# Kernel optimization log

Hardware: AMD Instinct MI355X
Metric: run time of the kernel (lower is better)

## Reference

```python
import jax, jax.numpy as jnp
import numpy as np

N = 100000
E = 1600000
D_IN = 128
D_H = 128


def setup_inputs() -> dict:
    key = jax.random.key(0)
    ks = jax.random.split(key, 8)
    x = jax.random.normal(ks[0], (N, D_IN), dtype=jnp.float32)
    edge_index = jax.random.randint(ks[1], (2, E), 0, N, dtype=jnp.int64)
    # Glorot-ish init for weights, zeros for biases (PyG GCNConv default: glorot W, zero bias)
    W1 = jax.random.normal(ks[2], (D_IN, D_H), dtype=jnp.float32) / np.sqrt(D_IN)
    b1 = jnp.zeros((D_H,), dtype=jnp.float32)
    W2 = jax.random.normal(ks[3], (D_H, D_H), dtype=jnp.float32) / np.sqrt(D_H)
    b2 = jnp.zeros((D_H,), dtype=jnp.float32)
    Wout = jax.random.normal(ks[4], (D_H, 1), dtype=jnp.float32) / np.sqrt(D_H)
    bout = jnp.zeros((1,), dtype=jnp.float32)
    return {"x": x, "edge_index": edge_index, "W1": W1, "b1": b1,
            "W2": W2, "b2": b2, "Wout": Wout, "bout": bout}


def _gcn_conv(x, W, b, src, dst, inv_sqrt_deg, inv_deg):
    # PyG GCNConv: h = x @ W; out = sum_{j in N(i)} norm_ij * h_j + (1/deg_i) * h_i + b
    # norm_ij = deg_i^-1/2 * deg_j^-1/2 with self-loops folded into deg.
    h = x @ W                                   # [N, D]
    norm = inv_sqrt_deg[src] * inv_sqrt_deg[dst]  # [E]
    msgs = h[src] * norm[:, None]               # [E, D] gather
    agg = jax.ops.segment_sum(msgs, dst, num_segments=x.shape[0])  # [N, D] scatter
    agg = agg + h * inv_deg[:, None]            # self-loop term (norm = 1/deg)
    return agg + b


def reference(x, edge_index, W1, b1, W2, b2, Wout, bout):
    src = edge_index[0]
    dst = edge_index[1]
    n = x.shape[0]
    # degree with self-loops: deg_i = 1 + #incoming edges to i
    deg = 1.0 + jax.ops.segment_sum(jnp.ones((src.shape[0],), dtype=x.dtype), dst, num_segments=n)
    inv_sqrt_deg = jax.lax.rsqrt(deg)
    inv_deg = 1.0 / deg
    h = jax.nn.relu(_gcn_conv(x, W1, b1, src, dst, inv_sqrt_deg, inv_deg))
    h = jax.nn.relu(_gcn_conv(h, W2, b2, src, dst, inv_sqrt_deg, inv_deg))
    logits = h @ Wout + bout                    # [N, 1]
    return jax.nn.sigmoid(logits).squeeze(-1)   # [N]
```

## Files before the change

kernel.cpp:

```cpp
#include <hip/hip_runtime.h>
#include <cstddef>

#define CAPD 64
#define BSZ 512
#define BSH 9
#define CHUNK 8192
#define BCAP 12288

typedef unsigned int uint;
typedef unsigned short ushort;
typedef unsigned char uchar;
typedef float f32x4 __attribute__((ext_vector_type(4)));
typedef _Float16 f16x8 __attribute__((ext_vector_type(8)));

__device__ inline float h_lo(uint v) {
    union { ushort u; _Float16 h; } c; c.u = (ushort)(v & 0xFFFFu); return (float)c.h;
}
__device__ inline float h_hi(uint v) {
    union { ushort u; _Float16 h; } c; c.u = (ushort)(v >> 16); return (float)c.h;
}
__device__ inline ushort h_bits(float x) {
    union { _Float16 h; ushort u; } c; c.h = (_Float16)x; return c.u;
}
__device__ inline uint h_pack(float a, float b) {
    return (uint)h_bits(a) | ((uint)h_bits(b) << 16);
}
__device__ inline float ub0(uint v) { return (float)(v & 0xFFu); }
__device__ inline float ub1(uint v) { return (float)((v >> 8) & 0xFFu); }
__device__ inline float ub2(uint v) { return (float)((v >> 16) & 0xFFu); }
__device__ inline float ub3(uint v) { return (float)(v >> 24); }

__global__ __launch_bounds__(256) void p3_scatter(const int* __restrict__ esrc,
                                                  const int* __restrict__ edst, int E,
                                                  int nb, int NB2,
                                                  int* __restrict__ bucketCursor,
                                                  unsigned* __restrict__ gSorted,
                                                  const float* __restrict__ W1,
                                                  const float* __restrict__ W2,
                                                  uint* __restrict__ Wt1,
                                                  uint* __restrict__ Wt2) {
    __shared__ __align__(16) char SHB[78848];
    int bid = blockIdx.x, tid = threadIdx.x;
    if (bid >= NB2) {
        const float* W = (bid - NB2) ? W2 : W1;
        uint* O = (bid - NB2) ? Wt2 : Wt1;
        float (*ws)[129] = (float(*)[129])SHB;
#pragma unroll
        for (int j = 0; j < 16; ++j) {
            int q = tid + 256 * j;
            int k = q >> 5, c = (q & 31) * 4;
            float4 v = *reinterpret_cast<const float4*>(W + k * 128 + c);
            ws[k][c] = v.x; ws[k][c + 1] = v.y; ws[k][c + 2] = v.z; ws[k][c + 3] = v.w;
        }
        __syncthreads();
#pragma unroll
        for (int j = 0; j < 32; ++j) {
            int q = tid + 256 * j;
            int ncol = q >> 6, kw = q & 63;
            O[q] = h_pack(ws[2 * kw][ncol], ws[2 * kw + 1][ncol]);
        }
        return;
    }
    uint*  payL = (uint*)SHB;
    uint*  outL = (uint*)(SHB + 32768);
    uchar* bktL = (uchar*)(SHB + 65536);
    int*   hist   = (int*)(SHB + 73728);
    int*   segoff = hist + 256;
    int*   cursor = segoff + 256;
    int*   gbase  = cursor + 256;
    int*   sc     = gbase + 256;
    int e0 = bid * CHUNK;
    int m = min(E - e0, CHUNK);
    for (int i = tid; i < m; i += 256) {
        unsigned d = (unsigned)edst[e0 + i];
        unsigned s = (unsigned)esrc[e0 + i];
        payL[i] = s | ((d & (BSZ - 1)) << 23);
        bktL[i] = (uchar)(d >> BSH);
    }
    hist[tid] = 0;
    __syncthreads();
    for (int i = tid; i < m; i += 256)
        atomicAdd(&hist[bktL[i]], 1);
    __syncthreads();
    sc[tid] = hist[tid];
    __syncthreads();
    for (int off = 1; off < 256; off <<= 1) {
        int v = (tid >= off) ? sc[tid - off] : 0;
        __syncthreads();
        sc[tid] += v;
        __syncthreads();
    }
    segoff[tid] = sc[tid] - hist[tid];
    cursor[tid] = segoff[tid];
    if (tid < nb && hist[tid] > 0) gbase[tid] = atomicAdd(&bucketCursor[tid], hist[tid]);
    __syncthreads();
    for (int i = tid; i < m; i += 256) {
        int b = (int)bktL[i];
        int p = atomicAdd(&cursor[b], 1);
        outL[p] = payL[i];
    }
    __syncthreads();
    int wave = tid >> 6, lane = tid & 63;
    for (int b = wave; b < nb; b += 4) {
        int off = segoff[b], len = hist[b];
        if (len == 0) continue;
        int gb = gbase[b];
        unsigned* dst = gSorted + (size_t)b * BCAP;
        for (int i = lane; i < len; i += 64)
            if (gb + i < BCAP) dst[gb + i] = outL[off + i];
    }
}

__global__ __launch_bounds__(256) void p4_build(const unsigned* __restrict__ gSorted,
                                                const int* __restrict__ bucketCursor,
                                                int nb, int N, int* __restrict__ cnt,
                                                float* __restrict__ isd,
                                                int* __restrict__ ell) {
    __shared__ unsigned ellL[128 * CAPD];
    __shared__ int cntL[128];
    int bid = blockIdx.x, tid = threadIdx.x;
    int bucket = bid >> 2;
    unsigned sub = (unsigned)(bid & 3);
    int n0 = bid * 128;
    int nValid = min(128, N - n0);
    if (nValid <= 0) return;
    for (int i = tid; i < 128; i += 256) cntL[i] = 0;
    __syncthreads();
    int len = bucketCursor[bucket];
    if (len > BCAP) len = BCAP;
    const unsigned* seg = gSorted + (size_t)bucket * BCAP;
    for (int i = tid; i < len; i += 256) {
        unsigned e = seg[i];
        unsigned dl = e >> 23;
        if ((dl >> 7) == sub) {
            int r = (int)(dl & 127u);
            int p = atomicAdd(&cntL[r], 1);
            if (p < CAPD) ellL[r * CAPD + p] = e & 0x7FFFFFu;
        }
    }
    __syncthreads();
    int total = nValid * CAPD;
    const int* ellLi = (const int*)ellL;
    for (int i = tid; i < total; i += 256) {
        int row = i >> 6, pos = i & 63;
        int c = cntL[row];
        if (pos < min(c, CAPD))
            ell[(size_t)n0 * CAPD + i] = ellLi[i];
    }
    for (int i = tid; i < nValid; i += 256) {
        int c = cntL[i];
        cnt[n0 + i] = c;
        isd[n0 + i] = rsqrtf(1.0f + (float)c);
    }
}

__device__ __forceinline__ void gemm_core(const void* __restrict__ A, int aF16,
                                          const uint* __restrict__ Wt,
                                          const float* __restrict__ scale,
                                          const float* __restrict__ isdT,
                                          uint* __restrict__ Tq,
                                          float* __restrict__ Ts,
                                          float* __restrict__ TscOut,
                                          int n, int m0, int tid, uint* SH) {
    char* shb = (char*)SH;
    if (aF16) {
        const uint* Af = (const uint*)A;
#pragma unroll
        for (int j = 0; j < 8; ++j) {
            int q = tid + 256 * j;
            int row = q >> 4, c16 = q & 15;
            int grow = m0 + row;
            uint4 v = make_uint4(0u, 0u, 0u, 0u);
            if (grow < n) v = *reinterpret_cast<const uint4*>(Af + (size_t)grow * 64 + c16 * 4);
            *reinterpret_cast<uint4*>(shb + row * 256 + ((c16 * 16) ^ ((row & 7) << 4))) = v;
        }
    } else {
        const float* Af = (const float*)A;
#pragma unroll
        for (int j = 0; j < 8; ++j) {
            int q = tid + 256 * j;
            int row = q >> 4, c16 = q & 15;
            int grow = m0 + row;
            uint4 o = make_uint4(0u, 0u, 0u, 0u);
            if (grow < n) {
                float4 v0 = *reinterpret_cast<const float4*>(Af + (size_t)grow * 128 + c16 * 8);
                float4 v1 = *reinterpret_cast<const float4*>(Af + (size_t)grow * 128 + c16 * 8 + 4);
                o.x = h_pack(v0.x, v0.y); o.y = h_pack(v0.z, v0.w);
                o.z = h_pack(v1.x, v1.y); o.w = h_pack(v1.z, v1.w);
            }
            *reinterpret_cast<uint4*>(shb + row * 256 + ((c16 * 16) ^ ((row & 7) << 4))) = o;
        }
    }
#pragma unroll
    for (int j = 0; j < 8; ++j) {
        int q = tid + 256 * j;
        int col = q >> 4, c16 = q & 15;
        uint4 v = *reinterpret_cast<const uint4*>(Wt + col * 64 + c16 * 4);
        *reinterpret_cast<uint4*>(shb + 32768 + col * 256 + ((c16 * 16) ^ ((col & 7) << 4))) = v;
    }
    __syncthreads();

    const int w = tid >> 6, l = tid & 63;
    const int lrow = l & 15, kg = l >> 4;
    const int swz = (lrow & 7) << 4;

    f32x4 acc[2][8] = {};
#pragma unroll
    for (int kk = 0; kk < 4; ++kk) {
        const int koff = (kk * 64 + kg * 16) ^ swz;
        f16x8 a[2], b[8];
#pragma unroll
        for (int mr = 0; mr < 2; ++mr) {
            int r = w * 32 + mr * 16 + lrow;
            a[mr] = *reinterpret_cast<const f16x8*>(shb + r * 256 + koff);
        }
#pragma unroll
        for (int nc = 0; nc < 8; ++nc) {
            int c = nc * 16 + lrow;
            b[nc] = *reinterpret_cast<const f16x8*>(shb + 32768 + c * 256 + koff);
        }
#pragma unroll
        for (int mr = 0; mr < 2; ++mr)
#pragma unroll
            for (int nc = 0; nc < 8; ++nc)
                acc[mr][nc] = __builtin_amdgcn_mfma_f32_16x16x32_f16(a[mr], b[nc], acc[mr][nc], 0, 0, 0);
    }
    __syncthreads();

    ushort* Cs = (ushort*)SH;
#pragma unroll
    for (int mr = 0; mr < 2; ++mr) {
        int rb = w * 32 + mr * 16 + kg * 4;
#pragma unroll
        for (int i = 0; i < 4; ++i) {
            int grow = m0 + rb + i;
            float s = scale ? ((grow < n) ? scale[grow] : 0.f) : 1.f;
#pragma unroll
            for (int nc = 0; nc < 8; ++nc)
                Cs[(rb + i) * 136 + nc * 16 + lrow] = h_bits(s * acc[mr][nc][i]);
        }
    }
    __syncthreads();
    const uint* Cw = (const uint*)SH;
#pragma unroll
    for (int j = 0; j < 8; ++j) {
        int q = tid + 256 * j;
        int row = q >> 4, c8 = q & 15;
        int grow = m0 + row;
        uint4 v = *reinterpret_cast<const uint4*>(Cw + row * 68 + c8 * 4);
        float f0 = h_lo(v.x), f1 = h_hi(v.x), f2 = h_lo(v.y), f3 = h_hi(v.y);
        float f4 = h_lo(v.z), f5 = h_hi(v.z), f6 = h_lo(v.w), f7 = h_hi(v.w);
        float mx = fmaxf(fmaxf(fmaxf(fabsf(f0), fabsf(f1)), fmaxf(fabsf(f2), fabsf(f3))),
                         fmaxf(fmaxf(fabsf(f4), fabsf(f5)), fmaxf(fabsf(f6), fabsf(f7))));
#pragma unroll
        for (int off = 8; off > 0; off >>= 1) mx = fmaxf(mx, __shfl_xor(mx, off, 16));
        mx = fmaxf(mx, 1e-20f);
        float inv = 127.f / mx;
        int q0 = (int)rintf(f0 * inv) + 128, q1 = (int)rintf(f1 * inv) + 128;
        int q2 = (int)rintf(f2 * inv) + 128, q3 = (int)rintf(f3 * inv) + 128;
        int q4 = (int)rintf(f4 * inv) + 128, q5 = (int)rintf(f5 * inv) + 128;
        int q6 = (int)rintf(f6 * inv) + 128, q7 = (int)rintf(f7 * inv) + 128;
        uint w0 = (uint)q0 | ((uint)q1 << 8) | ((uint)q2 << 16) | ((uint)q3 << 24);
        uint w1 = (uint)q4 | ((uint)q5 << 8) | ((uint)q6 << 16) | ((uint)q7 << 24);
        if (grow < n) {
            *reinterpret_cast<uint2*>(Tq + (size_t)grow * 32 + c8 * 2) = make_uint2(w0, w1);
            if (c8 == 0) {
                float ts = mx * (1.f / 127.f);
                Ts[grow] = ts;
                if (TscOut) TscOut[grow] = ts * isdT[grow];
            }
        }
    }
}

__global__ __launch_bounds__(256) void gemm1_kernel(const float* __restrict__ x,
                                                    const uint* __restrict__ Wt,
                                                    const float* __restrict__ isd,
                                                    uint* __restrict__ Tq,
                                                    float* __restrict__ Ts,
                                                    float* __restrict__ Tsc, int n) {
    __shared__ __align__(16) uint SH[16384];
    gemm_core(x, 0, Wt, nullptr, isd, Tq, Ts, Tsc, n, blockIdx.x * 128, threadIdx.x, SH);
}

__global__ __launch_bounds__(256) void gemm2_kernel(const uint* __restrict__ Hb,
                                                    const uint* __restrict__ Wt,
                                                    const float* __restrict__ isd,
                                                    uint* __restrict__ Tq,
                                                    float* __restrict__ Ts, int n) {
    __shared__ __align__(16) uint SH[16384];
    gemm_core(Hb, 1, Wt, isd, nullptr, Tq, Ts, nullptr, n, blockIdx.x * 128, threadIdx.x, SH);
}

__global__ __launch_bounds__(256) void agg_kernel(const uint* __restrict__ Tq,
                                                  const float* __restrict__ Tsc,
                                                  const int* __restrict__ ell,
                                                  const int* __restrict__ cnt,
                                                  const float* __restrict__ isd,
                                                  const float* __restrict__ bias,
                                                  uint* __restrict__ Hb, int n) {
    int node = (int)((blockIdx.x * 256 + threadIdx.x) >> 5);
    int ln = threadIdx.x & 31;
    if (node >= n) return;
    float di = isd[node];
    int c = cnt[node];
    if (c > CAPD) c = CAPD;
    const int* row = ell + (size_t)node * CAPD;
    float a0, a1, a2, a3, ssum;
    {
        uint v = Tq[(size_t)node * 32 + ln];
        float sc = Tsc[node];
        ssum = sc;
        a0 = sc * ub0(v); a1 = sc * ub1(v); a2 = sc * ub2(v); a3 = sc * ub3(v);
    }
    int j = 0;
    for (; j + 8 <= c; j += 8) {
        int4 sa = *reinterpret_cast<const int4*>(row + j);
        int4 sb = *reinterpret_cast<const int4*>(row + j + 4);
        uint v0 = Tq[(size_t)sa.x * 32 + ln]; float c0 = Tsc[sa.x];
        uint v1 = Tq[(size_t)sa.y * 32 + ln]; float c1 = Tsc[sa.y];
        uint v2 = Tq[(size_t)sa.z * 32 + ln]; float c2 = Tsc[sa.z];
        uint v3 = Tq[(size_t)sa.w * 32 + ln]; float c3 = Tsc[sa.w];
        uint v4 = Tq[(size_t)sb.x * 32 + ln]; float c4 = Tsc[sb.x];
        uint v5 = Tq[(size_t)sb.y * 32 + ln]; float c5 = Tsc[sb.y];
        uint v6 = Tq[(size_t)sb.z * 32 + ln]; float c6 = Tsc[sb.z];
        uint v7 = Tq[(size_t)sb.w * 32 + ln]; float c7 = Tsc[sb.w];
        ssum += ((c0 + c1) + (c2 + c3)) + ((c4 + c5) + (c6 + c7));
        a0 = fmaf(c0, ub0(v0), fmaf(c1, ub0(v1), fmaf(c2, ub0(v2), fmaf(c3, ub0(v3),
             fmaf(c4, ub0(v4), fmaf(c5, ub0(v5), fmaf(c6, ub0(v6), fmaf(c7, ub0(v7), a0))))))));
        a1 = fmaf(c0, ub1(v0), fmaf(c1, ub1(v1), fmaf(c2, ub1(v2), fmaf(c3, ub1(v3),
             fmaf(c4, ub1(v4), fmaf(c5, ub1(v5), fmaf(c6, ub1(v6), fmaf(c7, ub1(v7), a1))))))));
        a2 = fmaf(c0, ub2(v0), fmaf(c1, ub2(v1), fmaf(c2, ub2(v2), fmaf(c3, ub2(v3),
             fmaf(c4, ub2(v4), fmaf(c5, ub2(v5), fmaf(c6, ub2(v6), fmaf(c7, ub2(v7), a2))))))));
        a3 = fmaf(c0, ub3(v0), fmaf(c1, ub3(v1), fmaf(c2, ub3(v2), fmaf(c3, ub3(v3),
             fmaf(c4, ub3(v4), fmaf(c5, ub3(v5), fmaf(c6, ub3(v6), fmaf(c7, ub3(v7), a3))))))));
    }
    for (; j + 4 <= c; j += 4) {
        int4 s4 = *reinterpret_cast<const int4*>(row + j);
        uint v0 = Tq[(size_t)s4.x * 32 + ln]; float c0 = Tsc[s4.x];
        uint v1 = Tq[(size_t)s4.y * 32 + ln]; float c1 = Tsc[s4.y];
        uint v2 = Tq[(size_t)s4.z * 32 + ln]; float c2 = Tsc[s4.z];
        uint v3 = Tq[(size_t)s4.w * 32 + ln]; float c3 = Tsc[s4.w];
        ssum += (c0 + c1) + (c2 + c3);
        a0 = fmaf(c0, ub0(v0), fmaf(c1, ub0(v1), fmaf(c2, ub0(v2), fmaf(c3, ub0(v3), a0))));
        a1 = fmaf(c0, ub1(v0), fmaf(c1, ub1(v1), fmaf(c2, ub1(v2), fmaf(c3, ub1(v3), a1))));
        a2 = fmaf(c0, ub2(v0), fmaf(c1, ub2(v1), fmaf(c2, ub2(v2), fmaf(c3, ub2(v3), a2))));
        a3 = fmaf(c0, ub3(v0), fmaf(c1, ub3(v1), fmaf(c2, ub3(v2), fmaf(c3, ub3(v3), a3))));
    }
    for (; j < c; ++j) {
        int s = row[j];
        uint v = Tq[(size_t)s * 32 + ln];
        float sc = Tsc[s];
        ssum += sc;
        a0 = fmaf(sc, ub0(v), a0); a1 = fmaf(sc, ub1(v), a1);
        a2 = fmaf(sc, ub2(v), a2); a3 = fmaf(sc, ub3(v), a3);
    }
    float off = 128.f * ssum;
    float4 bv = *reinterpret_cast<const float4*>(bias + ln * 4);
    float h0 = fmaxf(fmaf(di, a0 - off, bv.x), 0.f);
    float h1 = fmaxf(fmaf(di, a1 - off, bv.y), 0.f);
    float h2 = fmaxf(fmaf(di, a2 - off, bv.z), 0.f);
    float h3 = fmaxf(fmaf(di, a3 - off, bv.w), 0.f);
    *reinterpret_cast<uint2*>(Hb + (size_t)node * 64 + ln * 2) =
        make_uint2(h_pack(h0, h1), h_pack(h2, h3));
}

__global__ __launch_bounds__(256) void agg_out_kernel(const uint* __restrict__ Tq,
                                                      const float* __restrict__ Ts,
                                                      const int* __restrict__ ell,
                                                      const int* __restrict__ cnt,
                                                      const float* __restrict__ isd,
                                                      const float* __restrict__ bias,
                                                      const float* __restrict__ Wout,
                                                      const float* __restrict__ bout,
                                                      float* __restrict__ out, int n) {
    int node = (int)((blockIdx.x * 256 + threadIdx.x) >> 5);
    int ln = threadIdx.x & 31;
    if (node >= n) return;
    float di = isd[node];
    int c = cnt[node];
    if (c > CAPD) c = CAPD;
    const int* row = ell + (size_t)node * CAPD;
    float a0, a1, a2, a3, ssum;
    {
        uint v = Tq[(size_t)node * 32 + ln];
        float sc = Ts[node];
        ssum = sc;
        a0 = sc * ub0(v); a1 = sc * ub1(v); a2 = sc * ub2(v); a3 = sc * ub3(v);
    }
    int j = 0;
    for (; j + 8 <= c; j += 8) {
        int4 sa = *reinterpret_cast<const int4*>(row + j);
        int4 sb = *reinterpret_cast<const int4*>(row + j + 4);
        uint v0 = Tq[(size_t)sa.x * 32 + ln]; float c0 = Ts[sa.x];
        uint v1 = Tq[(size_t)sa.y * 32 + ln]; float c1 = Ts[sa.y];
        uint v2 = Tq[(size_t)sa.z * 32 + ln]; float c2 = Ts[sa.z];
        uint v3 = Tq[(size_t)sa.w * 32 + ln]; float c3 = Ts[sa.w];
        uint v4 = Tq[(size_t)sb.x * 32 + ln]; float c4 = Ts[sb.x];
        uint v5 = Tq[(size_t)sb.y * 32 + ln]; float c5 = Ts[sb.y];
        uint v6 = Tq[(size_t)sb.z * 32 + ln]; float c6 = Ts[sb.z];
        uint v7 = Tq[(size_t)sb.w * 32 + ln]; float c7 = Ts[sb.w];
        ssum += ((c0 + c1) + (c2 + c3)) + ((c4 + c5) + (c6 + c7));
        a0 = fmaf(c0, ub0(v0), fmaf(c1, ub0(v1), fmaf(c2, ub0(v2), fmaf(c3, ub0(v3),
             fmaf(c4, ub0(v4), fmaf(c5, ub0(v5), fmaf(c6, ub0(v6), fmaf(c7, ub0(v7), a0))))))));
        a1 = fmaf(c0, ub1(v0), fmaf(c1, ub1(v1), fmaf(c2, ub1(v2), fmaf(c3, ub1(v3),
             fmaf(c4, ub1(v4), fmaf(c5, ub1(v5), fmaf(c6, ub1(v6), fmaf(c7, ub1(v7), a1))))))));
        a2 = fmaf(c0, ub2(v0), fmaf(c1, ub2(v1), fmaf(c2, ub2(v2), fmaf(c3, ub2(v3),
             fmaf(c4, ub2(v4), fmaf(c5, ub2(v5), fmaf(c6, ub2(v6), fmaf(c7, ub2(v7), a2))))))));
        a3 = fmaf(c0, ub3(v0), fmaf(c1, ub3(v1), fmaf(c2, ub3(v2), fmaf(c3, ub3(v3),
             fmaf(c4, ub3(v4), fmaf(c5, ub3(v5), fmaf(c6, ub3(v6), fmaf(c7, ub3(v7), a3))))))));
    }
    for (; j + 4 <= c; j += 4) {
        int4 s4 = *reinterpret_cast<const int4*>(row + j);
        uint v0 = Tq[(size_t)s4.x * 32 + ln]; float c0 = Ts[s4.x];
        uint v1 = Tq[(size_t)s4.y * 32 + ln]; float c1 = Ts[s4.y];
        uint v2 = Tq[(size_t)s4.z * 32 + ln]; float c2 = Ts[s4.z];
        uint v3 = Tq[(size_t)s4.w * 32 + ln]; float c3 = Ts[s4.w];
        ssum += (c0 + c1) + (c2 + c3);
        a0 = fmaf(c0, ub0(v0), fmaf(c1, ub0(v1), fmaf(c2, ub0(v2), fmaf(c3, ub0(v3), a0))));
        a1 = fmaf(c0, ub1(v0), fmaf(c1, ub1(v1), fmaf(c2, ub1(v2), fmaf(c3, ub1(v3), a1))));
        a2 = fmaf(c0, ub2(v0), fmaf(c1, ub2(v1), fmaf(c2, ub2(v2), fmaf(c3, ub2(v3), a2))));
        a3 = fmaf(c0, ub3(v0), fmaf(c1, ub3(v1), fmaf(c2, ub3(v2), fmaf(c3, ub3(v3), a3))));
    }
    for (; j < c; ++j) {
        int s = row[j];
        uint v = Tq[(size_t)s * 32 + ln];
        float sc = Ts[s];
        ssum += sc;
        a0 = fmaf(sc, ub0(v), a0); a1 = fmaf(sc, ub1(v), a1);
        a2 = fmaf(sc, ub2(v), a2); a3 = fmaf(sc, ub3(v), a3);
    }
    float off = 128.f * ssum;
    float4 bv = *reinterpret_cast<const float4*>(bias + ln * 4);
    float4 wv = *reinterpret_cast<const float4*>(Wout + ln * 4);
    float h0 = fmaxf(fmaf(di, a0 - off, bv.x), 0.f);
    float h1 = fmaxf(fmaf(di, a1 - off, bv.y), 0.f);
    float h2 = fmaxf(fmaf(di, a2 - off, bv.z), 0.f);
    float h3 = fmaxf(fmaf(di, a3 - off, bv.w), 0.f);
    float v = fmaf(h0, wv.x, fmaf(h1, wv.y, fmaf(h2, wv.z, h3 * wv.w)));
#pragma unroll
    for (int off2 = 16; off2 > 0; off2 >>= 1) v += __shfl_xor(v, off2, 32);
    if (ln == 0) out[node] = 1.f / (1.f + expf(-(v + bout[0])));
}

extern "C" void kernel_launch(void* const* d_in, const int* in_sizes, int n_in,
                              void* d_out, int out_size, void* d_ws, size_t ws_size,
                              hipStream_t stream) {
    const float* x    = (const float*)d_in[0];
    const int*   ei   = (const int*)d_in[1];
    const float* W1   = (const float*)d_in[2];
    const float* b1   = (const float*)d_in[3];
    const float* W2   = (const float*)d_in[4];
    const float* b2   = (const float*)d_in[5];
    const float* Wout = (const float*)d_in[6];
    const float* bout = (const float*)d_in[7];
    float* out = (float*)d_out;

    const int N = in_sizes[0] / 128;
    const int E = in_sizes[1] / 2;
    const int* esrc = ei;
    const int* edst = ei + E;

    char* p = (char*)d_ws;
    auto alloc = [&](size_t bytes) {
        char* r = p;
        p += (bytes + 255) & ~(size_t)255;
        return (void*)r;
    };
    const int nb  = (N + BSZ - 1) / BSZ;
    const int NB2 = (E + CHUNK - 1) / CHUNK;

    int*   cnt = (int*)  alloc((size_t)N * 4);
    float* isd = (float*)alloc((size_t)N * 4);
    int*   ell = (int*)  alloc((size_t)N * CAPD * 4);
    uint*  Tq  = (uint*) alloc((size_t)N * 32 * 4);
    float* Ts  = (float*)alloc((size_t)(N + 4) * 4);
    float* Tsc = (float*)alloc((size_t)(N + 4) * 4);
    uint*  Hb  = (uint*) alloc((size_t)N * 64 * 4);
    uint*  Wt1 = (uint*) alloc(8192 * 4);
    uint*  Wt2 = (uint*) alloc(8192 * 4);
    unsigned* gSorted      = (unsigned*)alloc((size_t)nb * BCAP * 4);
    int*      bucketCursor = (int*)     alloc((size_t)nb * 4);

    hipMemsetAsync(bucketCursor, 0, (size_t)nb * 4, stream);
    p3_scatter<<<NB2 + 2, 256, 0, stream>>>(esrc, edst, E, nb, NB2, bucketCursor, gSorted,
                                            W1, W2, Wt1, Wt2);
    p4_build<<<4 * nb, 256, 0, stream>>>(gSorted, bucketCursor, nb, N, cnt, isd, ell);

    const int gblocks = (N + 127) / 128;
    const int ablocks = (N + 7) / 8;
    gemm1_kernel<<<gblocks, 256, 0, stream>>>(x, Wt1, isd, Tq, Ts, Tsc, N);
    agg_kernel<<<ablocks, 256, 0, stream>>>(Tq, Tsc, ell, cnt, isd, b1, Hb, N);
    gemm2_kernel<<<gblocks, 256, 0, stream>>>(Hb, Wt2, isd, Tq, Ts, N);
    agg_out_kernel<<<ablocks, 256, 0, stream>>>(Tq, Ts, ell, cnt, isd, b2, Wout, bout, out, N);
}
```

Baseline: 188.5 us.

## Co-schedule layer-1 GEMM with edge bucketing and move isd scaling into build

The weight-transpose work and the bucket-cursor zeroing move into a small prep kernel, which replaces the memset. The first GEMM's blocks now run in the same grid as the edge-scatter blocks, so the compute-heavy GEMM can overlap the memory- and atomic-bound scatter. Because gemm1 no longer depends on isd, the Ts*isd product is now computed in p4_build. The change removes one launch and the serialization between the sort and the GEMM, at the cost of a bigger combined grid whose blocks reserve the larger shared-memory allocation.

Result: faster. 166.3 us (-11.7%).

```diff
diff --git a/kernel.cpp b/kernel.cpp
--- a/kernel.cpp
+++ b/kernel.cpp
@@ -30,35 +30,161 @@
 __device__ inline float ub2(uint v) { return (float)((v >> 16) & 0xFFu); }
 __device__ inline float ub3(uint v) { return (float)(v >> 24); }
 
-__global__ __launch_bounds__(256) void p3_scatter(const int* __restrict__ esrc,
-                                                  const int* __restrict__ edst, int E,
-                                                  int nb, int NB2,
-                                                  int* __restrict__ bucketCursor,
-                                                  unsigned* __restrict__ gSorted,
-                                                  const float* __restrict__ W1,
-                                                  const float* __restrict__ W2,
-                                                  uint* __restrict__ Wt1,
-                                                  uint* __restrict__ Wt2) {
+__global__ __launch_bounds__(256) void prep_kernel(int* __restrict__ bucketCursor, int nb,
+                                                   const float* __restrict__ W1,
+                                                   const float* __restrict__ W2,
+                                                   uint* __restrict__ Wt1,
+                                                   uint* __restrict__ Wt2) {
+    __shared__ float ws[128][129];
+    int bid = blockIdx.x, tid = threadIdx.x;
+    if (bid == 0) {
+        for (int i = tid; i < nb; i += 256) bucketCursor[i] = 0;
+        return;
+    }
+    const float* W = (bid == 2) ? W2 : W1;
+    uint* O = (bid == 2) ? Wt2 : Wt1;
+#pragma unroll
+    for (int j = 0; j < 16; ++j) {
+        int q = tid + 256 * j;
+        int k = q >> 5, c = (q & 31) * 4;
+        float4 v = *reinterpret_cast<const float4*>(W + k * 128 + c);
+        ws[k][c] = v.x; ws[k][c + 1] = v.y; ws[k][c + 2] = v.z; ws[k][c + 3] = v.w;
+    }
+    __syncthreads();
+#pragma unroll
+    for (int j = 0; j < 32; ++j) {
+        int q = tid + 256 * j;
+        int ncol = q >> 6, kw = q & 63;
+        O[q] = h_pack(ws[2 * kw][ncol], ws[2 * kw + 1][ncol]);
+    }
+}
+
+__device__ __forceinline__ void gemm_core(const void* __restrict__ A, int aF16,
+                                          const uint* __restrict__ Wt,
+                                          const float* __restrict__ scale,
+                                          uint* __restrict__ Tq,
+                                          float* __restrict__ Ts,
+                                          int n, int m0, int tid, uint* SH) {
+    char* shb = (char*)SH;
+    if (aF16) {
+        const uint* Af = (const uint*)A;
+#pragma unroll
+        for (int j = 0; j < 8; ++j) {
+            int q = tid + 256 * j;
+            int row = q >> 4, c16 = q & 15;
+            int grow = m0 + row;
+            uint4 v = make_uint4(0u, 0u, 0u, 0u);
+            if (grow < n) v = *reinterpret_cast<const uint4*>(Af + (size_t)grow * 64 + c16 * 4);
+            *reinterpret_cast<uint4*>(shb + row * 256 + ((c16 * 16) ^ ((row & 7) << 4))) = v;
+        }
+    } else {
+        const float* Af = (const float*)A;
+#pragma unroll
+        for (int j = 0; j < 8; ++j) {
+            int q = tid + 256 * j;
+            int row = q >> 4, c16 = q & 15;
+            int grow = m0 + row;
+            uint4 o = make_uint4(0u, 0u, 0u, 0u);
+            if (grow < n) {
+                float4 v0 = *reinterpret_cast<const float4*>(Af + (size_t)grow * 128 + c16 * 8);
+                float4 v1 = *reinterpret_cast<const float4*>(Af + (size_t)grow * 128 + c16 * 8 + 4);
+                o.x = h_pack(v0.x, v0.y); o.y = h_pack(v0.z, v0.w);
+                o.z = h_pack(v1.x, v1.y); o.w = h_pack(v1.z, v1.w);
+            }
+            *reinterpret_cast<uint4*>(shb + row * 256 + ((c16 * 16) ^ ((row & 7) << 4))) = o;
+        }
+    }
+#pragma unroll
+    for (int j = 0; j < 8; ++j) {
+        int q = tid + 256 * j;
+        int col = q >> 4, c16 = q & 15;
+        uint4 v = *reinterpret_cast<const uint4*>(Wt + col * 64 + c16 * 4);
+        *reinterpret_cast<uint4*>(shb + 32768 + col * 256 + ((c16 * 16) ^ ((col & 7) << 4))) = v;
+    }
+    __syncthreads();
+
+    const int w = tid >> 6, l = tid & 63;
+    const int lrow = l & 15, kg = l >> 4;
+    const int swz = (lrow & 7) << 4;
+
+    f32x4 acc[2][8] = {};
+#pragma unroll
+    for (int kk = 0; kk < 4; ++kk) {
+        const int koff = (kk * 64 + kg * 16) ^ swz;
+        f16x8 a[2], b[8];
+#pragma unroll
+        for (int mr = 0; mr < 2; ++mr) {
+            int r = w * 32 + mr * 16 + lrow;
+            a[mr] = *reinterpret_cast<const f16x8*>(shb + r * 256 + koff);
+        }
+#pragma unroll
+        for (int nc = 0; nc < 8; ++nc) {
+            int c = nc * 16 + lrow;
+            b[nc] = *reinterpret_cast<const f16x8*>(shb + 32768 + c * 256 + koff);
+        }
+#pragma unroll
+        for (int mr = 0; mr < 2; ++mr)
+#pragma unroll
+            for (int nc = 0; nc < 8; ++nc)
+                acc[mr][nc] = __builtin_amdgcn_mfma_f32_16x16x32_f16(a[mr], b[nc], acc[mr][nc], 0, 0, 0);
+    }
+    __syncthreads();
+
+    ushort* Cs = (ushort*)SH;
+#pragma unroll
+    for (int mr = 0; mr < 2; ++mr) {
+        int rb = w * 32 + mr * 16 + kg * 4;
+#pragma unroll
+        for (int i = 0; i < 4; ++i) {
+            int grow = m0 + rb + i;
+            float s = scale ? ((grow < n) ? scale[grow] : 0.f) : 1.f;
+#pragma unroll
+            for (int nc = 0; nc < 8; ++nc)
+                Cs[(rb + i) * 136 + nc * 16 + lrow] = h_bits(s * acc[mr][nc][i]);
+        }
+    }
+    __syncthreads();
+    const uint* Cw = (const uint*)SH;
+#pragma unroll
+    for (int j = 0; j < 8; ++j) {
+        int q = tid + 256 * j;
+        int row = q >> 4, c8 = q & 15;
+        int grow = m0 + row;
+        uint4 v = *reinterpret_cast<const uint4*>(Cw + row * 68 + c8 * 4);
+        float f0 = h_lo(v.x), f1 = h_hi(v.x), f2 = h_lo(v.y), f3 = h_hi(v.y);
+        float f4 = h_lo(v.z), f5 = h_hi(v.z), f6 = h_lo(v.w), f7 = h_hi(v.w);
+        float mx = fmaxf(fmaxf(fmaxf(fabsf(f0), fabsf(f1)), fmaxf(fabsf(f2), fabsf(f3))),
+                         fmaxf(fmaxf(fabsf(f4), fabsf(f5)), fmaxf(fabsf(f6), fabsf(f7))));
+#pragma unroll
+        for (int off = 8; off > 0; off >>= 1) mx = fmaxf(mx, __shfl_xor(mx, off, 16));
+        mx = fmaxf(mx, 1e-20f);
+        float inv = 127.f / mx;
+        int q0 = (int)rintf(f0 * inv) + 128, q1 = (int)rintf(f1 * inv) + 128;
+        int q2 = (int)rintf(f2 * inv) + 128, q3 = (int)rintf(f3 * inv) + 128;
+        int q4 = (int)rintf(f4 * inv) + 128, q5 = (int)rintf(f5 * inv) + 128;
+        int q6 = (int)rintf(f6 * inv) + 128, q7 = (int)rintf(f7 * inv) + 128;
+        uint w0 = (uint)q0 | ((uint)q1 << 8) | ((uint)q2 << 16) | ((uint)q3 << 24);
+        uint w1 = (uint)q4 | ((uint)q5 << 8) | ((uint)q6 << 16) | ((uint)q7 << 24);
+        if (grow < n) {
+            *reinterpret_cast<uint2*>(Tq + (size_t)grow * 32 + c8 * 2) = make_uint2(w0, w1);
+            if (c8 == 0) Ts[grow] = mx * (1.f / 127.f);
+        }
+    }
+}
+
+__global__ __launch_bounds__(256) void p3gemm1(const int* __restrict__ esrc,
+                                               const int* __restrict__ edst, int E,
+                                               int nb, int NB2,
+                                               int* __restrict__ bucketCursor,
+                                               unsigned* __restrict__ gSorted,
+                                               const float* __restrict__ x,
+                                               const uint* __restrict__ Wt1,
+                                               uint* __restrict__ Tq,
+                                               float* __restrict__ Ts, int N) {
     __shared__ __align__(16) char SHB[78848];
     int bid = blockIdx.x, tid = threadIdx.x;
     if (bid >= NB2) {
-        const float* W = (bid - NB2) ? W2 : W1;
-        uint* O = (bid - NB2) ? Wt2 : Wt1;
-        float (*ws)[129] = (float(*)[129])SHB;
-#pragma unroll
-        for (int j = 0; j < 16; ++j) {
-            int q = tid + 256 * j;
-            int k = q >> 5, c = (q & 31) * 4;
-            float4 v = *reinterpret_cast<const float4*>(W + k * 128 + c);
-            ws[k][c] = v.x; ws[k][c + 1] = v.y; ws[k][c + 2] = v.z; ws[k][c + 3] = v.w;
-        }
-        __syncthreads();
-#pragma unroll
-        for (int j = 0; j < 32; ++j) {
-            int q = tid + 256 * j;
-            int ncol = q >> 6, kw = q & 63;
-            O[q] = h_pack(ws[2 * kw][ncol], ws[2 * kw + 1][ncol]);
-        }
+        gemm_core(x, 0, Wt1, nullptr, Tq, Ts, N, (bid - NB2) * 128, tid, (uint*)SHB);
         return;
     }
     uint*  payL = (uint*)SHB;
@@ -115,7 +241,9 @@
                                                 const int* __restrict__ bucketCursor,
                                                 int nb, int N, int* __restrict__ cnt,
                                                 float* __restrict__ isd,
-                                                int* __restrict__ ell) {
+                                                int* __restrict__ ell,
+                                                const float* __restrict__ Ts,
+                                                float* __restrict__ Tsc) {
     __shared__ unsigned ellL[128 * CAPD];
     __shared__ int cntL[128];
     int bid = blockIdx.x, tid = threadIdx.x;
@@ -149,138 +277,11 @@
     }
     for (int i = tid; i < nValid; i += 256) {
         int c = cntL[i];
+        float iv = rsqrtf(1.0f + (float)c);
         cnt[n0 + i] = c;
-        isd[n0 + i] = rsqrtf(1.0f + (float)c);
-    }
-}
-
-__device__ __forceinline__ void gemm_core(const void* __restrict__ A, int aF16,
-                                          const uint* __restrict__ Wt,
-                                          const float* __restrict__ scale,
-                                          const float* __restrict__ isdT,
-                                          uint* __restrict__ Tq,
-                                          float* __restrict__ Ts,
-                                          float* __restrict__ TscOut,
-                                          int n, int m0, int tid, uint* SH) {
-    char* shb = (char*)SH;
-    if (aF16) {
-        const uint* Af = (const uint*)A;
-#pragma unroll
-        for (int j = 0; j < 8; ++j) {
-            int q = tid + 256 * j;
-            int row = q >> 4, c16 = q & 15;
-            int grow = m0 + row;
-            uint4 v = make_uint4(0u, 0u, 0u, 0u);
-            if (grow < n) v = *reinterpret_cast<const uint4*>(Af + (size_t)grow * 64 + c16 * 4);
-            *reinterpret_cast<uint4*>(shb + row * 256 + ((c16 * 16) ^ ((row & 7) << 4))) = v;
-        }
-    } else {
-        const float* Af = (const float*)A;
-#pragma unroll
-        for (int j = 0; j < 8; ++j) {
-            int q = tid + 256 * j;
-            int row = q >> 4, c16 = q & 15;
-            int grow = m0 + row;
-            uint4 o = make_uint4(0u, 0u, 0u, 0u);
-            if (grow < n) {
-                float4 v0 = *reinterpret_cast<const float4*>(Af + (size_t)grow * 128 + c16 * 8);
-                float4 v1 = *reinterpret_cast<const float4*>(Af + (size_t)grow * 128 + c16 * 8 + 4);
-                o.x = h_pack(v0.x, v0.y); o.y = h_pack(v0.z, v0.w);
-                o.z = h_pack(v1.x, v1.y); o.w = h_pack(v1.z, v1.w);
-            }
-            *reinterpret_cast<uint4*>(shb + row * 256 + ((c16 * 16) ^ ((row & 7) << 4))) = o;
-        }
-    }
-#pragma unroll
-    for (int j = 0; j < 8; ++j) {
-        int q = tid + 256 * j;
-        int col = q >> 4, c16 = q & 15;
-        uint4 v = *reinterpret_cast<const uint4*>(Wt + col * 64 + c16 * 4);
-        *reinterpret_cast<uint4*>(shb + 32768 + col * 256 + ((c16 * 16) ^ ((col & 7) << 4))) = v;
-    }
-    __syncthreads();
-
-    const int w = tid >> 6, l = tid & 63;
-    const int lrow = l & 15, kg = l >> 4;
-    const int swz = (lrow & 7) << 4;
-
-    f32x4 acc[2][8] = {};
-#pragma unroll
-    for (int kk = 0; kk < 4; ++kk) {
-        const int koff = (kk * 64 + kg * 16) ^ swz;
-        f16x8 a[2], b[8];
-#pragma unroll
-        for (int mr = 0; mr < 2; ++mr) {
-            int r = w * 32 + mr * 16 + lrow;
-            a[mr] = *reinterpret_cast<const f16x8*>(shb + r * 256 + koff);
-        }
-#pragma unroll
-        for (int nc = 0; nc < 8; ++nc) {
-            int c = nc * 16 + lrow;
-            b[nc] = *reinterpret_cast<const f16x8*>(shb + 32768 + c * 256 + koff);
-        }
-#pragma unroll
-        for (int mr = 0; mr < 2; ++mr)
-#pragma unroll
-            for (int nc = 0; nc < 8; ++nc)
-                acc[mr][nc] = __builtin_amdgcn_mfma_f32_16x16x32_f16(a[mr], b[nc], acc[mr][nc], 0, 0, 0);
-    }
-    __syncthreads();
-
-    ushort* Cs = (ushort*)SH;
-#pragma unroll
-    for (int mr = 0; mr < 2; ++mr) {
-        int rb = w * 32 + mr * 16 + kg * 4;
-#pragma unroll
-        for (int i = 0; i < 4; ++i) {
-            int grow = m0 + rb + i;
-            float s = scale ? ((grow < n) ? scale[grow] : 0.f) : 1.f;
-#pragma unroll
-            for (int nc = 0; nc < 8; ++nc)
-                Cs[(rb + i) * 136 + nc * 16 + lrow] = h_bits(s * acc[mr][nc][i]);
-        }
-    }
-    __syncthreads();
-    const uint* Cw = (const uint*)SH;
-#pragma unroll
-    for (int j = 0; j < 8; ++j) {
-        int q = tid + 256 * j;
-        int row = q >> 4, c8 = q & 15;
-        int grow = m0 + row;
-        uint4 v = *reinterpret_cast<const uint4*>(Cw + row * 68 + c8 * 4);
-        float f0 = h_lo(v.x), f1 = h_hi(v.x), f2 = h_lo(v.y), f3 = h_hi(v.y);
-        float f4 = h_lo(v.z), f5 = h_hi(v.z), f6 = h_lo(v.w), f7 = h_hi(v.w);
-        float mx = fmaxf(fmaxf(fmaxf(fabsf(f0), fabsf(f1)), fmaxf(fabsf(f2), fabsf(f3))),
-                         fmaxf(fmaxf(fabsf(f4), fabsf(f5)), fmaxf(fabsf(f6), fabsf(f7))));
-#pragma unroll
-        for (int off = 8; off > 0; off >>= 1) mx = fmaxf(mx, __shfl_xor(mx, off, 16));
-        mx = fmaxf(mx, 1e-20f);
-        float inv = 127.f / mx;
-        int q0 = (int)rintf(f0 * inv) + 128, q1 = (int)rintf(f1 * inv) + 128;
-        int q2 = (int)rintf(f2 * inv) + 128, q3 = (int)rintf(f3 * inv) + 128;
-        int q4 = (int)rintf(f4 * inv) + 128, q5 = (int)rintf(f5 * inv) + 128;
-        int q6 = (int)rintf(f6 * inv) + 128, q7 = (int)rintf(f7 * inv) + 128;
-        uint w0 = (uint)q0 | ((uint)q1 << 8) | ((uint)q2 << 16) | ((uint)q3 << 24);
-        uint w1 = (uint)q4 | ((uint)q5 << 8) | ((uint)q6 << 16) | ((uint)q7 << 24);
-        if (grow < n) {
-            *reinterpret_cast<uint2*>(Tq + (size_t)grow * 32 + c8 * 2) = make_uint2(w0, w1);
-            if (c8 == 0) {
-                float ts = mx * (1.f / 127.f);
-                Ts[grow] = ts;
-                if (TscOut) TscOut[grow] = ts * isdT[grow];
-            }
-        }
-    }
-}
-
-__global__ __launch_bounds__(256) void gemm1_kernel(const float* __restrict__ x,
-                                                    const uint* __restrict__ Wt,
-                                                    const float* __restrict__ isd,
-                                                    uint* __restrict__ Tq,
-                                                    float* __restrict__ Ts,
-                                                    float* __restrict__ Tsc, int n) {
-    __shared__ __align__(16) uint SH[16384];
-    gemm_core(x, 0, Wt, nullptr, isd, Tq, Ts, Tsc, n, blockIdx.x * 128, threadIdx.x, SH);
+        isd[n0 + i] = iv;
+        Tsc[n0 + i] = Ts[n0 + i] * iv;
+    }
 }
 
 __global__ __launch_bounds__(256) void gemm2_kernel(const uint* __restrict__ Hb,
@@ -289,7 +290,7 @@
                                                     uint* __restrict__ Tq,
                                                     float* __restrict__ Ts, int n) {
     __shared__ __align__(16) uint SH[16384];
-    gemm_core(Hb, 1, Wt, isd, nullptr, Tq, Ts, nullptr, n, blockIdx.x * 128, threadIdx.x, SH);
+    gemm_core(Hb, 1, Wt, isd, Tq, Ts, n, blockIdx.x * 128, threadIdx.x, SH);
 }
 
 __global__ __launch_bounds__(256) void agg_kernel(const uint* __restrict__ Tq,
@@ -482,14 +483,13 @@
     unsigned* gSorted      = (unsigned*)alloc((size_t)nb * BCAP * 4);
     int*      bucketCursor = (int*)     alloc((size_t)nb * 4);
 
-    hipMemsetAsync(bucketCursor, 0, (size_t)nb * 4, stream);
-    p3_scatter<<<NB2 + 2, 256, 0, stream>>>(esrc, edst, E, nb, NB2, bucketCursor, gSorted,
-                                            W1, W2, Wt1, Wt2);
-    p4_build<<<4 * nb, 256, 0, stream>>>(gSorted, bucketCursor, nb, N, cnt, isd, ell);
-
     const int gblocks = (N + 127) / 128;
     const int ablocks = (N + 7) / 8;
-    gemm1_kernel<<<gblocks, 256, 0, stream>>>(x, Wt1, isd, Tq, Ts, Tsc, N);
+
+    prep_kernel<<<3, 256, 0, stream>>>(bucketCursor, nb, W1, W2, Wt1, Wt2);
+    p3gemm1<<<NB2 + gblocks, 256, 0, stream>>>(esrc, edst, E, nb, NB2, bucketCursor,
+                                               gSorted, x, Wt1, Tq, Ts, N);
+    p4_build<<<4 * nb, 256, 0, stream>>>(gSorted, bucketCursor, nb, N, cnt, isd, ell, Ts, Tsc);
     agg_kernel<<<ablocks, 256, 0, stream>>>(Tq, Tsc, ell, cnt, isd, b1, Hb, N);
     gemm2_kernel<<<gblocks, 256, 0, stream>>>(Hb, Wt2, isd, Tq, Ts, N);
     agg_out_kernel<<<ablocks, 256, 0, stream>>>(Tq, Ts, ell, cnt, isd, b2, Wout, bout, out, N);
```
